# Optimization experiments

Hardware: AMD Instinct MI355X
Metric: run time of the kernel (lower is better)

## Reference

```python
import jax, jax.numpy as jnp
import numpy as np
import math

B, N, CS, CZ, H, C, P, PV, NB = 1, 512, 384, 128, 12, 16, 4, 8, 64


def quat_to_rot(q):
    q = q / jnp.clip(jnp.linalg.norm(q, axis=-1, keepdims=True), 1e-8)
    w, x, y, z = q[..., 0], q[..., 1], q[..., 2], q[..., 3]
    return jnp.stack([
        w*w + x*x - y*y - z*z, 2*(x*y - w*z), 2*(x*z + w*y),
        2*(x*y + w*z), w*w - x*x + y*y - z*z, 2*(y*z - w*x),
        2*(x*z - w*y), 2*(y*z + w*x), w*w - x*x - y*y + z*z,
    ], axis=-1).reshape(q.shape[:-1] + (3, 3))


def setup_inputs() -> dict:
    key = jax.random.key(0)
    ks = jax.random.split(key, 28)
    def n(k, shape, sc=1.0):
        return jax.random.normal(k, shape, jnp.float32) * sc
    s = n(ks[0], (B, N, CS))
    z = n(ks[1], (B, N, N, CZ))
    translations = n(ks[2], (B, N, 3)) * 4.0  # spread distances over 0-32A bins
    rotations = quat_to_rot(n(ks[3], (B, N, 4)))  # valid SO(3) frames
    mask = jnp.ones((B, N), dtype=bool)
    inv = lambda fan: 1.0 / math.sqrt(fan)
    return {
        's': s, 'z': z, 'translations': translations, 'rotations': rotations, 'mask': mask,
        'Wq': n(ks[4], (CS, H*C), inv(CS)), 'bq': n(ks[5], (H*C,), 0.01),
        'Wk': n(ks[6], (CS, H*C), inv(CS)), 'bk': n(ks[7], (H*C,), 0.01),
        'Wv': n(ks[8], (CS, H*C), inv(CS)), 'bv': n(ks[9], (H*C,), 0.01),
        'Wqp': n(ks[10], (CS, H*P*3), inv(CS)), 'bqp': n(ks[11], (H*P*3,), 0.01),
        'Wkp': n(ks[12], (CS, H*P*3), inv(CS)), 'bkp': n(ks[13], (H*P*3,), 0.01),
        'Wvp': n(ks[14], (CS, H*PV*3), inv(CS)), 'bvp': n(ks[15], (H*PV*3,), 0.01),
        'Wb': n(ks[16], (CZ, H), inv(CZ)), 'bb': n(ks[17], (H,), 0.01),
        'dist_emb': n(ks[18], (NB, H), 0.02),
        'scale_logits': n(ks[19], (3, H), 0.1),
        'head_weights': jnp.abs(n(ks[20], (H,))) * 0.2 + 0.8,
        'Wout': n(ks[21], (H*(C + PV*4 + CZ), CS), inv(H*(C + PV*4 + CZ))),
        'bout': n(ks[22], (CS,), 0.01),
    }


def reference(s, z, translations, rotations, mask, Wq, bq, Wk, bk, Wv, bv,
              Wqp, bqp, Wkp, bkp, Wvp, bvp, Wb, bb, dist_emb, scale_logits,
              head_weights, Wout, bout):
    b, n, _ = s.shape
    q = (s @ Wq + bq).reshape(b, n, H, C)
    k = (s @ Wk + bk).reshape(b, n, H, C)
    v = (s @ Wv + bv).reshape(b, n, H, C)
    q_pts = (s @ Wqp + bqp).reshape(b, n, H, P, 3)
    k_pts = (s @ Wkp + bkp).reshape(b, n, H, P, 3)
    v_pts = (s @ Wvp + bvp).reshape(b, n, H, PV, 3)
    t = translations[:, :, None, None, :]
    q_g = jnp.einsum('bnij,bnhpj->bnhpi', rotations, q_pts) + t
    k_g = jnp.einsum('bnij,bnhpj->bnhpi', rotations, k_pts) + t
    v_g = jnp.einsum('bnij,bnhpj->bnhpi', rotations, v_pts) + t
    scalar_logits = jnp.einsum('bnhc,bmhc->bnmh', q, k) / math.sqrt(C)
    # squared point distances, summed over points p and coords i, via expansion
    q_sq = (q_g**2).sum((-1, -2))  # (b, n, h)
    k_sq = (k_g**2).sum((-1, -2))
    cross = jnp.einsum('bnhpi,bmhpi->bnmh', q_g, k_g)
    point_dist = q_sq[:, :, None, :] + k_sq[:, None, :, :] - 2.0 * cross
    point_logits = -0.5 * point_dist * head_weights
    pair_bias = z @ Wb + bb  # (b, n, m, h)
    pair_dist = jnp.linalg.norm(
        translations[:, :, None, :] - translations[:, None, :, :], axis=-1)
    edges = jnp.linspace(0.0, 32.0, NB + 1)
    bins = jnp.clip(jnp.searchsorted(edges, pair_dist, side='left') - 1, 0, NB - 1)
    dist_bias = dist_emb[bins]
    local = (pair_dist <= 5.0).astype(s.dtype)
    medium = ((pair_dist > 5.0) & (pair_dist <= 15.0)).astype(s.dtype)
    scales = jnp.stack([local, medium, jnp.ones_like(pair_dist)], axis=-1)
    per_head = jax.nn.softmax(scale_logits, axis=0)  # (3, h)
    multiscale = jnp.einsum('bnms,sh->bnmh', scales, per_head)
    logits = scalar_logits + point_logits + pair_bias + dist_bias + multiscale
    m2d = mask[:, :, None] & mask[:, None, :]
    logits = jnp.where(m2d[..., None], logits, -10000.0)
    attn = jax.nn.softmax(logits.astype(jnp.float32), axis=2).astype(s.dtype)
    out_scalar = jnp.einsum('bnmh,bmhc->bnhc', attn, v)
    out_pts_g = jnp.einsum('bnmh,bmhpi->bnhpi', attn, v_g)
    out_pts_l = jnp.einsum('bnji,bnhpj->bnhpi', rotations, out_pts_g - t)  # R^T x
    out_norms = jnp.linalg.norm(out_pts_l, axis=-1)  # (b, n, h, pv)
    pair_feat = jnp.einsum('bnmh,bnmc->bnhc', attn, z)
    feats = jnp.concatenate(
        [out_scalar, out_pts_l.reshape(b, n, H, PV * 3), out_norms, pair_feat],
        axis=-1).reshape(b, n, -1)
    return feats @ Wout + bout
```

## Files before the change

### kernel.cpp

```cpp
#include <hip/hip_runtime.h>
#include <math.h>

#define N   512
#define CS  384
#define CZ  128
#define H   12
#define C   16
#define P   4
#define PV  8
#define NB  64
#define KSP 528
#define QKD 28
#define QPAD 68
#define APAD 516

#define OFF_Q    0
#define OFF_K    98304
#define OFF_V    196608
#define OFF_QP   294912
#define OFF_KP   368640
#define OFF_VP   442368
#define OFF_QG   589824
#define OFF_KG   663552
#define OFF_VG   737280
#define OFF_QSQ  884736
#define OFF_KSQ  890880
#define OFF_LOG  897024
#define OFF_FEAT 4042752

__global__ __launch_bounds__(256) void k_proj(
    const float* __restrict__ s,
    const float* __restrict__ Wq,  const float* __restrict__ bq,
    const float* __restrict__ Wk,  const float* __restrict__ bk,
    const float* __restrict__ Wv,  const float* __restrict__ bv,
    const float* __restrict__ Wqp, const float* __restrict__ bqp,
    const float* __restrict__ Wkp, const float* __restrict__ bkp,
    const float* __restrict__ Wvp, const float* __restrict__ bvp,
    float* __restrict__ ws)
{
    __shared__ float s_s[16*388];
    __shared__ float part[4*16*68];
    const int tid = threadIdx.x;
    const int n0  = blockIdx.y * 16;
    const int cq  = tid & 15;
    const int rg  = (tid >> 4) & 3;
    const int ks  = tid >> 6;
    const int gc  = blockIdx.x * 64 + cq * 4;
    for (int i = tid; i < 16*384; i += 256) {
        int r = i / 384, c = i - r*384;
        s_s[r*388 + c] = s[(n0 + r)*384 + c];
    }
    __syncthreads();
    const float* W; int width; int lc;
    if      (gc < 192) { W=Wq;  width=192; lc=gc;     }
    else if (gc < 384) { W=Wk;  width=192; lc=gc-192; }
    else if (gc < 576) { W=Wv;  width=192; lc=gc-384; }
    else if (gc < 720) { W=Wqp; width=144; lc=gc-576; }
    else if (gc < 864) { W=Wkp; width=144; lc=gc-720; }
    else               { W=Wvp; width=288; lc=gc-864; }
    float acc[4][4] = {{0.f}};
    const float* wp   = W + lc + (size_t)(ks*96)*width;
    const float* srow = s_s + (rg*4)*388 + ks*96;
    #pragma unroll 4
    for (int kk = 0; kk < 96; kk++) {
        float4 w4 = *(const float4*)(wp + (size_t)kk*width);
        #pragma unroll
        for (int r = 0; r < 4; r++) {
            float sv = srow[r*388 + kk];
            acc[r][0] += sv*w4.x; acc[r][1] += sv*w4.y;
            acc[r][2] += sv*w4.z; acc[r][3] += sv*w4.w;
        }
    }
    #pragma unroll
    for (int r = 0; r < 4; r++)
        *(float4*)(part + (ks*16 + rg*4 + r)*68 + cq*4) =
            make_float4(acc[r][0], acc[r][1], acc[r][2], acc[r][3]);
    __syncthreads();
    {
        const int row = tid >> 4;
        float4 sum = *(const float4*)(part + (0*16 + row)*68 + cq*4);
        #pragma unroll
        for (int k2 = 1; k2 < 4; k2++) {
            float4 p = *(const float4*)(part + (k2*16 + row)*68 + cq*4);
            sum.x += p.x; sum.y += p.y; sum.z += p.z; sum.w += p.w;
        }
        const float* b; float* dst; int w2, lc2;
        if      (gc < 192) { b=bq;  w2=192; lc2=gc;     dst=ws+OFF_Q;  }
        else if (gc < 384) { b=bk;  w2=192; lc2=gc-192; dst=ws+OFF_K;  }
        else if (gc < 576) { b=bv;  w2=192; lc2=gc-384; dst=ws+OFF_V;  }
        else if (gc < 720) { b=bqp; w2=144; lc2=gc-576; dst=ws+OFF_QP; }
        else if (gc < 864) { b=bkp; w2=144; lc2=gc-720; dst=ws+OFF_KP; }
        else               { b=bvp; w2=288; lc2=gc-864; dst=ws+OFF_VP; }
        float4 b4 = *(const float4*)(b + lc2);
        sum.x += b4.x; sum.y += b4.y; sum.z += b4.z; sum.w += b4.w;
        *(float4*)(dst + (size_t)(n0+row)*w2 + lc2) = sum;
    }
}

__global__ __launch_bounds__(192) void k_frames(
    const float* __restrict__ rot, const float* __restrict__ trans,
    float* __restrict__ ws)
{
    int n = blockIdx.x, tid = threadIdx.x;
    __shared__ float R[9], T[3], qg_s[144], kg_s[144];
    if (tid < 9) R[tid] = rot[n*9 + tid];
    if (tid < 3) T[tid] = trans[n*3 + tid];
    __syncthreads();
    if (tid < 48) {
        const float* lp = ws + OFF_QP + n*144 + tid*3;
        float l0=lp[0], l1=lp[1], l2=lp[2];
        float* gp = ws + OFF_QG + n*144 + tid*3;
        for (int i=0;i<3;i++){ float g = R[i*3+0]*l0 + R[i*3+1]*l1 + R[i*3+2]*l2 + T[i]; gp[i]=g; qg_s[tid*3+i]=g; }
    } else if (tid < 96) {
        int u = tid-48;
        const float* lp = ws + OFF_KP + n*144 + u*3;
        float l0=lp[0], l1=lp[1], l2=lp[2];
        float* gp = ws + OFF_KG + n*144 + u*3;
        for (int i=0;i<3;i++){ float g = R[i*3+0]*l0 + R[i*3+1]*l1 + R[i*3+2]*l2 + T[i]; gp[i]=g; kg_s[u*3+i]=g; }
    } else {
        int u = tid-96;
        const float* lp = ws + OFF_VP + n*288 + u*3;
        float l0=lp[0], l1=lp[1], l2=lp[2];
        float* gp = ws + OFF_VG + n*288 + u*3;
        for (int i=0;i<3;i++){ float g = R[i*3+0]*l0 + R[i*3+1]*l1 + R[i*3+2]*l2 + T[i]; gp[i]=g; }
    }
    __syncthreads();
    if (tid < 12) {
        float a=0;
        for (int d=0; d<12; d++){ float x=qg_s[tid*12+d]; a+=x*x; }
        ws[OFF_QSQ + n*12 + tid]=a;
    } else if (tid < 24) {
        int h = tid-12; float a=0;
        for (int d=0; d<12; d++){ float x=kg_s[h*12+d]; a+=x*x; }
        ws[OFF_KSQ + n*12 + h]=a;
    }
}

__global__ __launch_bounds__(256) void k_qkpt(
    const float* __restrict__ head_weights, float* __restrict__ ws)
{
    __shared__ float qs[QKD*QPAD], ks[QKD*QPAD], qa[64], kb[64];
    const int tid = threadIdx.x;
    const int m0 = blockIdx.x * 64, n0 = blockIdx.y * 64, h = blockIdx.z;
    const float hw = head_weights[h];
    for (int idx = tid; idx < 64*16; idx += 256) {
        int r = idx >> 4, c = idx & 15;
        qs[c*QPAD + r] = ws[OFF_Q + (n0+r)*192 + h*16 + c] * 0.25f;
        ks[c*QPAD + r] = ws[OFF_K + (m0+r)*192 + h*16 + c];
    }
    for (int idx = tid; idx < 64*12; idx += 256) {
        int r = idx / 12, c = idx % 12;
        qs[(16+c)*QPAD + r] = ws[OFF_QG + (n0+r)*144 + h*12 + c] * hw;
        ks[(16+c)*QPAD + r] = ws[OFF_KG + (m0+r)*144 + h*12 + c];
    }
    for (int idx = tid; idx < 64; idx += 256) {
        qa[idx] = -0.5f * hw * ws[OFF_QSQ + (n0+idx)*12 + h];
        kb[idx] = -0.5f * hw * ws[OFF_KSQ + (m0+idx)*12 + h];
    }
    __syncthreads();
    const int tx = tid & 15, ty = tid >> 4;
    float acc[4][4] = {{0.f}};
    #pragma unroll 4
    for (int d = 0; d < QKD; d++) {
        float4 a = *(const float4*)(qs + d*QPAD + ty*4);
        float4 b = *(const float4*)(ks + d*QPAD + tx*4);
        const float* ap = &a.x; const float* bp = &b.x;
        #pragma unroll
        for (int i=0;i<4;i++)
            #pragma unroll
            for (int j=0;j<4;j++) acc[i][j] += ap[i]*bp[j];
    }
    #pragma unroll
    for (int i=0;i<4;i++) {
        float ai = qa[ty*4+i];
        float4 r;
        r.x = acc[i][0] + ai + kb[tx*4+0];
        r.y = acc[i][1] + ai + kb[tx*4+1];
        r.z = acc[i][2] + ai + kb[tx*4+2];
        r.w = acc[i][3] + ai + kb[tx*4+3];
        *(float4*)(ws + OFF_LOG + ((size_t)(n0+ty*4+i)*H + h)*N + m0 + tx*4) = r;
    }
}

__global__ __launch_bounds__(256) void k_zbias(
    const float* __restrict__ z, const float* __restrict__ trans,
    const float* __restrict__ Wb, const float* __restrict__ bb,
    const float* __restrict__ dist_emb, const float* __restrict__ scale_logits,
    float* __restrict__ ws)
{
    const int n = blockIdx.y;
    const int m = blockIdx.x * 256 + threadIdx.x;
    float dx = trans[n*3+0]-trans[m*3+0];
    float dy = trans[n*3+1]-trans[m*3+1];
    float dz = trans[n*3+2]-trans[m*3+2];
    float pd = sqrtf(dx*dx+dy*dy+dz*dz);
    int bin = (int)ceilf(2.f*pd) - 1;
    bin = bin < 0 ? 0 : (bin > NB-1 ? NB-1 : bin);
    const float4 de0 = *(const float4*)(dist_emb + bin*12);
    const float4 de1 = *(const float4*)(dist_emb + bin*12 + 4);
    const float4 de2 = *(const float4*)(dist_emb + bin*12 + 8);
    float de[12] = {de0.x,de0.y,de0.z,de0.w, de1.x,de1.y,de1.z,de1.w, de2.x,de2.y,de2.z,de2.w};
    float acc[12];
    #pragma unroll
    for (int h=0; h<12; h++) {
        float a = scale_logits[0*H+h], b = scale_logits[1*H+h], c = scale_logits[2*H+h];
        float mx = fmaxf(a, fmaxf(b,c));
        float ea=__expf(a-mx), eb=__expf(b-mx), ec=__expf(c-mx);
        float inv = 1.f/(ea+eb+ec);
        float msc = ec*inv;
        if (pd <= 5.f)       msc += ea*inv;
        else if (pd <= 15.f) msc += eb*inv;
        acc[h] = bb[h] + de[h] + msc;
    }
    const float* zp = z + ((size_t)n*N + m)*CZ;
    #pragma unroll 2
    for (int c4 = 0; c4 < CZ/4; c4++) {
        float4 z4 = *(const float4*)(zp + c4*4);
        const float* zv = &z4.x;
        #pragma unroll
        for (int j=0; j<4; j++)
            #pragma unroll
            for (int h=0; h<12; h++)
                acc[h] += zv[j] * Wb[(c4*4+j)*H + h];
    }
    float* lp = ws + OFF_LOG + (size_t)n*H*N + m;
    #pragma unroll
    for (int h=0; h<12; h++)
        lp[(size_t)h*N] += acc[h];
}

__global__ __launch_bounds__(256) void k_pairz(
    const float* __restrict__ z, float* __restrict__ ws)
{
    __shared__ float attn_s[H*APAD];
    __shared__ float part[4*12*64];
    const int ch = blockIdx.x, n = blockIdx.y;
    const int tid = threadIdx.x;
    const int lane = tid & 63, wave = tid >> 6;

    const float4* asrc = (const float4*)(ws + OFF_LOG + (size_t)n*H*N);
    for (int i = tid; i < H*(N/4); i += 256) {
        int h = i >> 7, q = i & 127;
        *(float4*)(attn_s + h*APAD + q*4) = asrc[h*128 + q];
    }
    __syncthreads();
    for (int h = wave; h < H; h += 4) {
        float* row = attn_s + h*APAD;
        float v[8]; float mx = -1e30f;
        #pragma unroll
        for (int j=0;j<8;j++){ v[j]=row[lane + j*64]; mx = fmaxf(mx, v[j]); }
        #pragma unroll
        for (int off=32; off>0; off>>=1) mx = fmaxf(mx, __shfl_xor(mx, off, 64));
        float sum = 0.f;
        #pragma unroll
        for (int j=0;j<8;j++){ v[j]=__expf(v[j]-mx); sum += v[j]; }
        #pragma unroll
        for (int off=32; off>0; off>>=1) sum += __shfl_xor(sum, off, 64);
        float inv = 1.f/sum;
        #pragma unroll
        for (int j=0;j<8;j++) row[lane + j*64] = v[j]*inv;
    }
    __syncthreads();

    const int cq = tid & 15;
    const int ms = tid >> 4;
    const float* zb = z + (size_t)n*N*CZ + ch*64 + cq*4;
    float4 acc[12];
    #pragma unroll
    for (int h=0; h<12; h++) acc[h] = make_float4(0.f,0.f,0.f,0.f);
    const int r0 = ms*32;
    #pragma unroll 2
    for (int rq = 0; rq < 8; rq++) {
        const int r = r0 + rq*4;
        float4 z0 = *(const float4*)(zb + (size_t)(r+0)*CZ);
        float4 z1 = *(const float4*)(zb + (size_t)(r+1)*CZ);
        float4 z2 = *(const float4*)(zb + (size_t)(r+2)*CZ);
        float4 z3 = *(const float4*)(zb + (size_t)(r+3)*CZ);
        #pragma unroll
        for (int h=0; h<12; h++) {
            float4 a4 = *(const float4*)(attn_s + h*APAD + r);
            acc[h].x += a4.x*z0.x + a4.y*z1.x + a4.z*z2.x + a4.w*z3.x;
            acc[h].y += a4.x*z0.y + a4.y*z1.y + a4.z*z2.y + a4.w*z3.y;
            acc[h].z += a4.x*z0.z + a4.y*z1.z + a4.z*z2.z + a4.w*z3.z;
            acc[h].w += a4.x*z0.w + a4.y*z1.w + a4.z*z2.w + a4.w*z3.w;
        }
    }
    #pragma unroll
    for (int h=0; h<12; h++) {
        acc[h].x += __shfl_xor(acc[h].x, 16, 64); acc[h].y += __shfl_xor(acc[h].y, 16, 64);
        acc[h].z += __shfl_xor(acc[h].z, 16, 64); acc[h].w += __shfl_xor(acc[h].w, 16, 64);
        acc[h].x += __shfl_xor(acc[h].x, 32, 64); acc[h].y += __shfl_xor(acc[h].y, 32, 64);
        acc[h].z += __shfl_xor(acc[h].z, 32, 64); acc[h].w += __shfl_xor(acc[h].w, 32, 64);
    }
    if (lane < 16) {
        #pragma unroll
        for (int h=0; h<12; h++)
            *(float4*)(part + (wave*12 + h)*64 + lane*4) = acc[h];
    }
    __syncthreads();
    if (tid < 192) {
        const int h = tid >> 4, c4 = tid & 15;
        float4 s = *(const float4*)(part + (0*12 + h)*64 + c4*4);
        #pragma unroll
        for (int w=1; w<4; w++) {
            float4 p = *(const float4*)(part + (w*12 + h)*64 + c4*4);
            s.x += p.x; s.y += p.y; s.z += p.z; s.w += p.w;
        }
        *(float4*)(ws + OFF_FEAT + (size_t)n*2112 + h*176 + 48 + ch*64 + c4*4) = s;
    }
}

__global__ __launch_bounds__(256) void k_attnA(
    const float* __restrict__ rot, const float* __restrict__ trans,
    float* __restrict__ ws)
{
    __shared__ float attn_s[H*APAD];
    __shared__ float part[240*4];
    __shared__ float og_s[288];
    const int n = blockIdx.x, tid = threadIdx.x;
    const int lane = tid & 63, wave = tid >> 6;

    const float4* asrc = (const float4*)(ws + OFF_LOG + (size_t)n*H*N);
    for (int i = tid; i < H*(N/4); i += 256) {
        int h = i >> 7, q = i & 127;
        *(float4*)(attn_s + h*APAD + q*4) = asrc[h*128 + q];
    }
    __syncthreads();
    for (int h = wave; h < H; h += 4) {
        float* row = attn_s + h*APAD;
        float v[8]; float mx = -1e30f;
        #pragma unroll
        for (int j=0;j<8;j++){ v[j]=row[lane + j*64]; mx = fmaxf(mx, v[j]); }
        #pragma unroll
        for (int off=32; off>0; off>>=1) mx = fmaxf(mx, __shfl_xor(mx, off, 64));
        float sum = 0.f;
        #pragma unroll
        for (int j=0;j<8;j++){ v[j]=__expf(v[j]-mx); sum += v[j]; }
        #pragma unroll
        for (int off=32; off>0; off>>=1) sum += __shfl_xor(sum, off, 64);
        float inv = 1.f/sum;
        #pragma unroll
        for (int j=0;j<8;j++) row[lane + j*64] = v[j]*inv;
    }
    __syncthreads();

    if (tid < 240) {
        const int col4 = (tid % 120) * 4;
        const int msA  = tid / 120;
        const float* aptr; int astride, ah;
        if (col4 < 192) { ah = col4 >> 4;        aptr = ws + OFF_V  + col4;       astride = 192; }
        else            { ah = (col4-192) / 24;  aptr = ws + OFF_VG + (col4-192); astride = 288; }
        const float4* arow = (const float4*)(attn_s + ah*APAD);
        float4 acc = {0.f,0.f,0.f,0.f};
        #pragma unroll 2
        for (int mq = msA*64; mq < msA*64 + 64; mq++) {
            float4 a4 = arow[mq];
            const float* vp = aptr + (size_t)mq*4*astride;
            float4 v0 = *(const float4*)(vp);
            float4 v1 = *(const float4*)(vp + astride);
            float4 v2 = *(const float4*)(vp + 2*astride);
            float4 v3 = *(const float4*)(vp + 3*astride);
            acc.x += a4.x*v0.x + a4.y*v1.x + a4.z*v2.x + a4.w*v3.x;
            acc.y += a4.x*v0.y + a4.y*v1.y + a4.z*v2.y + a4.w*v3.y;
            acc.z += a4.x*v0.z + a4.y*v1.z + a4.z*v2.z + a4.w*v3.z;
            acc.w += a4.x*v0.w + a4.y*v1.w + a4.z*v2.w + a4.w*v3.w;
        }
        *(float4*)(part + tid*4) = acc;
    }
    __syncthreads();
    if (tid < 120) {
        const int col4 = tid * 4;
        float4 a = *(const float4*)(part + tid*4);
        float4 b = *(const float4*)(part + (tid+120)*4);
        a.x += b.x; a.y += b.y; a.z += b.z; a.w += b.w;
        if (col4 < 192) {
            const int ah = col4 >> 4;
            *(float4*)(ws + OFF_FEAT + (size_t)n*2112 + ah*176 + (col4 & 15)) = a;
        } else {
            *(float4*)(og_s + (col4 - 192)) = a;
        }
    }
    __syncthreads();
    if (tid < 96) {
        const int h = tid >> 3, p = tid & 7;
        float g0 = og_s[h*24 + p*3 + 0] - trans[n*3+0];
        float g1 = og_s[h*24 + p*3 + 1] - trans[n*3+1];
        float g2 = og_s[h*24 + p*3 + 2] - trans[n*3+2];
        const float* R = rot + n*9;
        float* fdst = ws + OFF_FEAT + (size_t)n*2112 + h*176;
        float nsq = 0.f;
        #pragma unroll
        for (int i=0;i<3;i++){
            float l = R[0*3+i]*g0 + R[1*3+i]*g1 + R[2*3+i]*g2;
            fdst[16 + p*3 + i] = l;
            nsq += l*l;
        }
        fdst[40 + p] = sqrtf(nsq);
    }
}

__global__ __launch_bounds__(384) void k_bias(
    const float* __restrict__ bout, float* __restrict__ out)
{
    out[(size_t)blockIdx.x*CS + threadIdx.x] = bout[threadIdx.x];
}

__global__ __launch_bounds__(256) void k_out(
    const float* __restrict__ Wout, const float* __restrict__ ws,
    float* __restrict__ out)
{
    __shared__ float f_s[16*KSP];
    __shared__ float part[4*16*68];
    const int tid = threadIdx.x;
    const int n0  = blockIdx.y * 16;
    const int k0  = blockIdx.z * KSP;
    const int cq  = tid & 15;
    const int rg  = (tid >> 4) & 3;
    const int ks  = tid >> 6;
    const int col = blockIdx.x * 64 + cq * 4;
    for (int i = tid; i < 16*KSP; i += 256) {
        int r = i / KSP, c = i - r*KSP;
        f_s[i] = ws[OFF_FEAT + (size_t)(n0 + r)*2112 + k0 + c];
    }
    __syncthreads();
    float acc[4][4] = {{0.f}};
    const float* wp = Wout + (size_t)(k0 + ks*132)*CS + col;
    const float* f0 = f_s + (rg*4)*KSP + ks*132;
    #pragma unroll 4
    for (int kk = 0; kk < 132; kk++) {
        float4 w4 = *(const float4*)(wp + (size_t)kk*CS);
        #pragma unroll
        for (int r = 0; r < 4; r++) {
            float fv = f0[r*KSP + kk];
            acc[r][0] += fv*w4.x; acc[r][1] += fv*w4.y;
            acc[r][2] += fv*w4.z; acc[r][3] += fv*w4.w;
        }
    }
    #pragma unroll
    for (int r = 0; r < 4; r++)
        *(float4*)(part + (ks*16 + rg*4 + r)*68 + cq*4) =
            make_float4(acc[r][0], acc[r][1], acc[r][2], acc[r][3]);
    __syncthreads();
    {
        const int row = tid >> 4;
        float4 s = *(const float4*)(part + (0*16 + row)*68 + cq*4);
        #pragma unroll
        for (int k2 = 1; k2 < 4; k2++) {
            float4 p = *(const float4*)(part + (k2*16 + row)*68 + cq*4);
            s.x += p.x; s.y += p.y; s.z += p.z; s.w += p.w;
        }
        float* o = out + (size_t)(n0+row)*CS + col;
        atomicAdd(o+0, s.x); atomicAdd(o+1, s.y);
        atomicAdd(o+2, s.z); atomicAdd(o+3, s.w);
    }
}

extern "C" void kernel_launch(void* const* d_in, const int* in_sizes, int n_in,
                              void* d_out, int out_size, void* d_ws, size_t ws_size,
                              hipStream_t stream) {
    const float* s     = (const float*)d_in[0];
    const float* z     = (const float*)d_in[1];
    const float* trans = (const float*)d_in[2];
    const float* rot   = (const float*)d_in[3];
    const float* Wq  = (const float*)d_in[5];  const float* bq  = (const float*)d_in[6];
    const float* Wk  = (const float*)d_in[7];  const float* bk  = (const float*)d_in[8];
    const float* Wv  = (const float*)d_in[9];  const float* bv  = (const float*)d_in[10];
    const float* Wqp = (const float*)d_in[11]; const float* bqp = (const float*)d_in[12];
    const float* Wkp = (const float*)d_in[13]; const float* bkp = (const float*)d_in[14];
    const float* Wvp = (const float*)d_in[15]; const float* bvp = (const float*)d_in[16];
    const float* Wb  = (const float*)d_in[17]; const float* bb  = (const float*)d_in[18];
    const float* dist_emb     = (const float*)d_in[19];
    const float* scale_logits = (const float*)d_in[20];
    const float* head_weights = (const float*)d_in[21];
    const float* Wout = (const float*)d_in[22]; const float* bout = (const float*)d_in[23];
    float* out = (float*)d_out;
    float* ws  = (float*)d_ws;

    k_proj<<<dim3(18, 32), 256, 0, stream>>>(s, Wq,bq, Wk,bk, Wv,bv, Wqp,bqp, Wkp,bkp, Wvp,bvp, ws);
    k_frames<<<N, 192, 0, stream>>>(rot, trans, ws);
    k_qkpt<<<dim3(8, 8, 12), 256, 0, stream>>>(head_weights, ws);
    k_zbias<<<dim3(2, 512), 256, 0, stream>>>(z, trans, Wb, bb, dist_emb, scale_logits, ws);
    k_pairz<<<dim3(2, 512), 256, 0, stream>>>(z, ws);
    k_attnA<<<N, 256, 0, stream>>>(rot, trans, ws);
    k_bias<<<N, CS, 0, stream>>>(bout, out);
    k_out<<<dim3(6, 32, 4), 256, 0, stream>>>(Wout, ws, out);
}
```

Baseline: 368.8 us.

## Fuse z-bias, pair-feature and attention kernels into one per-row kernel

Measured after the change: 344.2 us. -6.7%, faster.

```diff
diff --git a/kernel.cpp b/kernel.cpp
--- a/kernel.cpp
+++ b/kernel.cpp
@@ -182,60 +182,17 @@
     }
 }
 
-__global__ __launch_bounds__(256) void k_zbias(
+__global__ __launch_bounds__(256) void k_attn_all(
     const float* __restrict__ z, const float* __restrict__ trans,
+    const float* __restrict__ rot,
     const float* __restrict__ Wb, const float* __restrict__ bb,
     const float* __restrict__ dist_emb, const float* __restrict__ scale_logits,
     float* __restrict__ ws)
 {
-    const int n = blockIdx.y;
-    const int m = blockIdx.x * 256 + threadIdx.x;
-    float dx = trans[n*3+0]-trans[m*3+0];
-    float dy = trans[n*3+1]-trans[m*3+1];
-    float dz = trans[n*3+2]-trans[m*3+2];
-    float pd = sqrtf(dx*dx+dy*dy+dz*dz);
-    int bin = (int)ceilf(2.f*pd) - 1;
-    bin = bin < 0 ? 0 : (bin > NB-1 ? NB-1 : bin);
-    const float4 de0 = *(const float4*)(dist_emb + bin*12);
-    const float4 de1 = *(const float4*)(dist_emb + bin*12 + 4);
-    const float4 de2 = *(const float4*)(dist_emb + bin*12 + 8);
-    float de[12] = {de0.x,de0.y,de0.z,de0.w, de1.x,de1.y,de1.z,de1.w, de2.x,de2.y,de2.z,de2.w};
-    float acc[12];
-    #pragma unroll
-    for (int h=0; h<12; h++) {
-        float a = scale_logits[0*H+h], b = scale_logits[1*H+h], c = scale_logits[2*H+h];
-        float mx = fmaxf(a, fmaxf(b,c));
-        float ea=__expf(a-mx), eb=__expf(b-mx), ec=__expf(c-mx);
-        float inv = 1.f/(ea+eb+ec);
-        float msc = ec*inv;
-        if (pd <= 5.f)       msc += ea*inv;
-        else if (pd <= 15.f) msc += eb*inv;
-        acc[h] = bb[h] + de[h] + msc;
-    }
-    const float* zp = z + ((size_t)n*N + m)*CZ;
-    #pragma unroll 2
-    for (int c4 = 0; c4 < CZ/4; c4++) {
-        float4 z4 = *(const float4*)(zp + c4*4);
-        const float* zv = &z4.x;
-        #pragma unroll
-        for (int j=0; j<4; j++)
-            #pragma unroll
-            for (int h=0; h<12; h++)
-                acc[h] += zv[j] * Wb[(c4*4+j)*H + h];
-    }
-    float* lp = ws + OFF_LOG + (size_t)n*H*N + m;
-    #pragma unroll
-    for (int h=0; h<12; h++)
-        lp[(size_t)h*N] += acc[h];
-}
-
-__global__ __launch_bounds__(256) void k_pairz(
-    const float* __restrict__ z, float* __restrict__ ws)
-{
     __shared__ float attn_s[H*APAD];
     __shared__ float part[4*12*64];
-    const int ch = blockIdx.x, n = blockIdx.y;
-    const int tid = threadIdx.x;
+    __shared__ float og_s[288];
+    const int n = blockIdx.x, tid = threadIdx.x;
     const int lane = tid & 63, wave = tid >> 6;
 
     const float4* asrc = (const float4*)(ws + OFF_LOG + (size_t)n*H*N);
@@ -244,6 +201,49 @@
         *(float4*)(attn_s + h*APAD + q*4) = asrc[h*128 + q];
     }
     __syncthreads();
+
+    const float tnx = trans[n*3+0], tny = trans[n*3+1], tnz = trans[n*3+2];
+    for (int half = 0; half < 2; half++) {
+        const int m = tid + half*256;
+        float dx = tnx - trans[m*3+0];
+        float dy = tny - trans[m*3+1];
+        float dz = tnz - trans[m*3+2];
+        float pd = sqrtf(dx*dx+dy*dy+dz*dz);
+        int bin = (int)ceilf(2.f*pd) - 1;
+        bin = bin < 0 ? 0 : (bin > NB-1 ? NB-1 : bin);
+        const float4 de0 = *(const float4*)(dist_emb + bin*12);
+        const float4 de1 = *(const float4*)(dist_emb + bin*12 + 4);
+        const float4 de2 = *(const float4*)(dist_emb + bin*12 + 8);
+        float de[12] = {de0.x,de0.y,de0.z,de0.w, de1.x,de1.y,de1.z,de1.w, de2.x,de2.y,de2.z,de2.w};
+        float acc[12];
+        #pragma unroll
+        for (int h=0; h<12; h++) {
+            float sa = scale_logits[0*H+h], sb = scale_logits[1*H+h], sc = scale_logits[2*H+h];
+            float mx = fmaxf(sa, fmaxf(sb,sc));
+            float ea=__expf(sa-mx), eb=__expf(sb-mx), ec=__expf(sc-mx);
+            float inv = 1.f/(ea+eb+ec);
+            float msc = ec*inv;
+            if (pd <= 5.f)       msc += ea*inv;
+            else if (pd <= 15.f) msc += eb*inv;
+            acc[h] = bb[h] + de[h] + msc;
+        }
+        const float* zp = z + ((size_t)n*N + m)*CZ;
+        #pragma unroll 2
+        for (int c4 = 0; c4 < CZ/4; c4++) {
+            float4 z4 = *(const float4*)(zp + c4*4);
+            const float* zv = &z4.x;
+            #pragma unroll
+            for (int j=0; j<4; j++)
+                #pragma unroll
+                for (int h=0; h<12; h++)
+                    acc[h] += zv[j] * Wb[(c4*4+j)*H + h];
+        }
+        #pragma unroll
+        for (int h=0; h<12; h++)
+            attn_s[h*APAD + m] += acc[h];
+    }
+    __syncthreads();
+
     for (int h = wave; h < H; h += 4) {
         float* row = attn_s + h*APAD;
         float v[8]; float mx = -1e30f;
@@ -264,85 +264,53 @@
 
     const int cq = tid & 15;
     const int ms = tid >> 4;
-    const float* zb = z + (size_t)n*N*CZ + ch*64 + cq*4;
-    float4 acc[12];
-    #pragma unroll
-    for (int h=0; h<12; h++) acc[h] = make_float4(0.f,0.f,0.f,0.f);
-    const int r0 = ms*32;
-    #pragma unroll 2
-    for (int rq = 0; rq < 8; rq++) {
-        const int r = r0 + rq*4;
-        float4 z0 = *(const float4*)(zb + (size_t)(r+0)*CZ);
-        float4 z1 = *(const float4*)(zb + (size_t)(r+1)*CZ);
-        float4 z2 = *(const float4*)(zb + (size_t)(r+2)*CZ);
-        float4 z3 = *(const float4*)(zb + (size_t)(r+3)*CZ);
+    for (int ch = 0; ch < 2; ch++) {
+        const float* zb = z + (size_t)n*N*CZ + ch*64 + cq*4;
+        float4 acc[12];
+        #pragma unroll
+        for (int h=0; h<12; h++) acc[h] = make_float4(0.f,0.f,0.f,0.f);
+        const int r0 = ms*32;
+        #pragma unroll 2
+        for (int rq = 0; rq < 8; rq++) {
+            const int r = r0 + rq*4;
+            float4 z0 = *(const float4*)(zb + (size_t)(r+0)*CZ);
+            float4 z1 = *(const float4*)(zb + (size_t)(r+1)*CZ);
+            float4 z2 = *(const float4*)(zb + (size_t)(r+2)*CZ);
+            float4 z3 = *(const float4*)(zb + (size_t)(r+3)*CZ);
+            #pragma unroll
+            for (int h=0; h<12; h++) {
+                float4 a4 = *(const float4*)(attn_s + h*APAD + r);
+                acc[h].x += a4.x*z0.x + a4.y*z1.x + a4.z*z2.x + a4.w*z3.x;
+                acc[h].y += a4.x*z0.y + a4.y*z1.y + a4.z*z2.y + a4.w*z3.y;
+                acc[h].z += a4.x*z0.z + a4.y*z1.z + a4.z*z2.z + a4.w*z3.z;
+                acc[h].w += a4.x*z0.w + a4.y*z1.w + a4.z*z2.w + a4.w*z3.w;
+            }
+        }
         #pragma unroll
         for (int h=0; h<12; h++) {
-            float4 a4 = *(const float4*)(attn_s + h*APAD + r);
-            acc[h].x += a4.x*z0.x + a4.y*z1.x + a4.z*z2.x + a4.w*z3.x;
-            acc[h].y += a4.x*z0.y + a4.y*z1.y + a4.z*z2.y + a4.w*z3.y;
-            acc[h].z += a4.x*z0.z + a4.y*z1.z + a4.z*z2.z + a4.w*z3.z;
-            acc[h].w += a4.x*z0.w + a4.y*z1.w + a4.z*z2.w + a4.w*z3.w;
-        }
-    }
-    #pragma unroll
-    for (int h=0; h<12; h++) {
-        acc[h].x += __shfl_xor(acc[h].x, 16, 64); acc[h].y += __shfl_xor(acc[h].y, 16, 64);
-        acc[h].z += __shfl_xor(acc[h].z, 16, 64); acc[h].w += __shfl_xor(acc[h].w, 16, 64);
-        acc[h].x += __shfl_xor(acc[h].x, 32, 64); acc[h].y += __shfl_xor(acc[h].y, 32, 64);
-        acc[h].z += __shfl_xor(acc[h].z, 32, 64); acc[h].w += __shfl_xor(acc[h].w, 32, 64);
-    }
-    if (lane < 16) {
-        #pragma unroll
-        for (int h=0; h<12; h++)
-            *(float4*)(part + (wave*12 + h)*64 + lane*4) = acc[h];
-    }
-    __syncthreads();
-    if (tid < 192) {
-        const int h = tid >> 4, c4 = tid & 15;
-        float4 s = *(const float4*)(part + (0*12 + h)*64 + c4*4);
-        #pragma unroll
-        for (int w=1; w<4; w++) {
-            float4 p = *(const float4*)(part + (w*12 + h)*64 + c4*4);
-            s.x += p.x; s.y += p.y; s.z += p.z; s.w += p.w;
-        }
-        *(float4*)(ws + OFF_FEAT + (size_t)n*2112 + h*176 + 48 + ch*64 + c4*4) = s;
-    }
-}
-
-__global__ __launch_bounds__(256) void k_attnA(
-    const float* __restrict__ rot, const float* __restrict__ trans,
-    float* __restrict__ ws)
-{
-    __shared__ float attn_s[H*APAD];
-    __shared__ float part[240*4];
-    __shared__ float og_s[288];
-    const int n = blockIdx.x, tid = threadIdx.x;
-    const int lane = tid & 63, wave = tid >> 6;
-
-    const float4* asrc = (const float4*)(ws + OFF_LOG + (size_t)n*H*N);
-    for (int i = tid; i < H*(N/4); i += 256) {
-        int h = i >> 7, q = i & 127;
-        *(float4*)(attn_s + h*APAD + q*4) = asrc[h*128 + q];
-    }
-    __syncthreads();
-    for (int h = wave; h < H; h += 4) {
-        float* row = attn_s + h*APAD;
-        float v[8]; float mx = -1e30f;
-        #pragma unroll
-        for (int j=0;j<8;j++){ v[j]=row[lane + j*64]; mx = fmaxf(mx, v[j]); }
-        #pragma unroll
-        for (int off=32; off>0; off>>=1) mx = fmaxf(mx, __shfl_xor(mx, off, 64));
-        float sum = 0.f;
-        #pragma unroll
-        for (int j=0;j<8;j++){ v[j]=__expf(v[j]-mx); sum += v[j]; }
-        #pragma unroll
-        for (int off=32; off>0; off>>=1) sum += __shfl_xor(sum, off, 64);
-        float inv = 1.f/sum;
-        #pragma unroll
-        for (int j=0;j<8;j++) row[lane + j*64] = v[j]*inv;
-    }
-    __syncthreads();
+            acc[h].x += __shfl_xor(acc[h].x, 16, 64); acc[h].y += __shfl_xor(acc[h].y, 16, 64);
+            acc[h].z += __shfl_xor(acc[h].z, 16, 64); acc[h].w += __shfl_xor(acc[h].w, 16, 64);
+            acc[h].x += __shfl_xor(acc[h].x, 32, 64); acc[h].y += __shfl_xor(acc[h].y, 32, 64);
+            acc[h].z += __shfl_xor(acc[h].z, 32, 64); acc[h].w += __shfl_xor(acc[h].w, 32, 64);
+        }
+        if (lane < 16) {
+            #pragma unroll
+            for (int h=0; h<12; h++)
+                *(float4*)(part + (wave*12 + h)*64 + lane*4) = acc[h];
+        }
+        __syncthreads();
+        if (tid < 192) {
+            const int h = tid >> 4, c4 = tid & 15;
+            float4 s4 = *(const float4*)(part + (0*12 + h)*64 + c4*4);
+            #pragma unroll
+            for (int w=1; w<4; w++) {
+                float4 p = *(const float4*)(part + (w*12 + h)*64 + c4*4);
+                s4.x += p.x; s4.y += p.y; s4.z += p.z; s4.w += p.w;
+            }
+            *(float4*)(ws + OFF_FEAT + (size_t)n*2112 + h*176 + 48 + ch*64 + c4*4) = s4;
+        }
+        __syncthreads();
+    }
 
     if (tid < 240) {
         const int col4 = (tid % 120) * 4;
@@ -479,9 +447,7 @@
     k_proj<<<dim3(18, 32), 256, 0, stream>>>(s, Wq,bq, Wk,bk, Wv,bv, Wqp,bqp, Wkp,bkp, Wvp,bvp, ws);
     k_frames<<<N, 192, 0, stream>>>(rot, trans, ws);
     k_qkpt<<<dim3(8, 8, 12), 256, 0, stream>>>(head_weights, ws);
-    k_zbias<<<dim3(2, 512), 256, 0, stream>>>(z, trans, Wb, bb, dist_emb, scale_logits, ws);
-    k_pairz<<<dim3(2, 512), 256, 0, stream>>>(z, ws);
-    k_attnA<<<N, 256, 0, stream>>>(rot, trans, ws);
+    k_attn_all<<<N, 256, 0, stream>>>(z, trans, rot, Wb, bb, dist_emb, scale_logits, ws);
     k_bias<<<N, CS, 0, stream>>>(bout, out);
     k_out<<<dim3(6, 32, 4), 256, 0, stream>>>(Wout, ws, out);
 }
```
